# Kernel tuning notes

Measured on AMD Instinct MI355X. Metric: run time of the kernel, lower is better.

The kernel has to match this reference:

```python
import jax, jax.numpy as jnp
import numpy as np
import math

B, T, C = 4, 2048, 1024
N = 16
D = C // N  # 64
SCALE = 1.0 / math.sqrt(C)  # weight init scale, matches 1/sqrt(in_features)


def setup_inputs() -> dict:
    key = jax.random.key(0)
    ks = jax.random.split(key, 5)
    x = jax.random.normal(ks[0], (B, T, C), dtype=jnp.float32)
    wq = jax.random.normal(ks[1], (C, C), dtype=jnp.float32) * SCALE
    wk = jax.random.normal(ks[2], (C, C), dtype=jnp.float32) * SCALE
    wv = jax.random.normal(ks[3], (C, C), dtype=jnp.float32) * SCALE
    wp = jax.random.normal(ks[4], (C, C), dtype=jnp.float32) * SCALE
    zb = jnp.zeros((C,), dtype=jnp.float32)
    return {"x": x, "wq": wq, "bq": zb, "wk": wk, "bk": zb,
            "wv": wv, "bv": zb, "wp": wp, "bp": zb}


def reference(x, wq, bq, wk, bk, wv, bv, wp, bp):
    # q/k/v projections (torch Linear: x @ W.T + b), split into heads
    q = (x @ wq.T + bq).reshape(B, T, N, D)
    k = (x @ wk.T + bk).reshape(B, T, N, D)
    v = (x @ wv.T + bv).reshape(B, T, N, D)
    # scores [B, N, T, T] with causal mask (include_query=True -> key_dim = T)
    scores = jnp.einsum('bqnd,bknd->bnqk', q, k) / math.sqrt(D)
    causal = jnp.tril(jnp.ones((T, T), dtype=bool))
    scores = jnp.where(causal[None, None], scores, -jnp.inf)
    probs = jax.nn.softmax(scores, axis=-1)
    # attention output, clamp to [-10, 10] (drop_p = 0, head_mask = None)
    attn = jnp.einsum('bnqk,bknd->bqnd', probs, v)
    attn = jnp.clip(attn, -10.0, 10.0).reshape(B, T, C)
    out = attn @ wp.T + bp
    out = jnp.clip(out, -10.0, 10.0)
    return out
```

## Files before the change

### kernel.cpp

```cpp
#include <hip/hip_runtime.h>
#include <stdint.h>

typedef __attribute__((ext_vector_type(4))) float f32x4;
typedef __attribute__((ext_vector_type(8))) _Float16 h8;
typedef __attribute__((ext_vector_type(4))) float f4v;
typedef __attribute__((ext_vector_type(4))) _Float16 h4v;

#define B_ 4
#define T_ 2048
#define C_ 1024
#define NH 16
#define HD 64
#define M_ (B_*T_)
#define KD 1024

#define MFMA16(a, b, c) __builtin_amdgcn_mfma_f32_16x16x32_f16(a, b, c, 0, 0, 0)

#define GL2LDS16(g, l) \
  __builtin_amdgcn_global_load_lds((const __attribute__((address_space(1))) unsigned int*)(g), \
      (__attribute__((address_space(3))) unsigned int*)(unsigned int)(uintptr_t)(l), 16, 0, 0)

__global__ void cast_x_kernel(const float* __restrict__ src, _Float16* __restrict__ dst, int n4) {
  int i = blockIdx.x * blockDim.x + threadIdx.x;
  if (i < n4) {
    f4v v = ((const f4v*)src)[i];
    ((h4v*)dst)[i] = __builtin_convertvector(v, h4v);
  }
}

__device__ __forceinline__ void stage_f32_128x32(const float* src, _Float16* dst, int lane, int wav) {
  #pragma unroll
  for (int hh = 0; hh < 2; hh++) {
    int row = hh*64 + wav*16 + (lane >> 2);
    int colf = (lane & 3) * 8;
    const float* p = src + (size_t)row * KD + colf;
    f4v a = *(const f4v*)p;
    f4v b = *(const f4v*)(p + 4);
    h8 v;
    v[0]=(_Float16)a[0]; v[1]=(_Float16)a[1]; v[2]=(_Float16)a[2]; v[3]=(_Float16)a[3];
    v[4]=(_Float16)b[0]; v[5]=(_Float16)b[1]; v[6]=(_Float16)b[2]; v[7]=(_Float16)b[3];
    *(h8*)(dst + row*32 + colf) = v;
  }
}

template<int AMODE>
__global__ __launch_bounds__(256) void gemm_qkv_kernel(
    const _Float16* __restrict__ Xh, const float* __restrict__ Xf,
    const float* __restrict__ Wq, const float* __restrict__ Wk, const float* __restrict__ Wv,
    const float* __restrict__ bq, const float* __restrict__ bk, const float* __restrict__ bv,
    _Float16* __restrict__ Qo, _Float16* __restrict__ Ko, _Float16* __restrict__ Vo)
{
  __shared__ _Float16 As[128*32];
  __shared__ _Float16 Bs[128*32];
  int tid = threadIdx.x;
  int lane = tid & 63, wav = tid >> 6;
  int mb = blockIdx.x;
  int nbg = blockIdx.y;
  int sel = nbg >> 3, nb = nbg & 7;
  const float* W = sel == 0 ? Wq : (sel == 1 ? Wk : Wv);
  const float* bias = sel == 0 ? bq : (sel == 1 ? bk : bv);
  _Float16* Out = sel == 0 ? Qo : (sel == 1 ? Ko : Vo);
  int m0 = mb * 128, n0 = nb * 128;

  f32x4 acc[4][4] = {};

  int r_in = lane >> 2;
  int c8   = (lane & 3) * 8;
  int l15 = lane & 15, l4 = lane >> 4;
  int wr = (wav >> 1) * 64, wc = (wav & 1) * 64;

  for (int k0 = 0; k0 < KD; k0 += 32) {
    if (AMODE == 0) {
      GL2LDS16(Xh + (size_t)(m0 +      wav*16 + r_in)*KD + k0 + c8, As +        wav*512);
      GL2LDS16(Xh + (size_t)(m0 + 64 + wav*16 + r_in)*KD + k0 + c8, As + 2048 + wav*512);
    } else {
      stage_f32_128x32(Xf + (size_t)m0 * KD + k0, As, lane, wav);
    }
    stage_f32_128x32(W + (size_t)n0 * KD + k0, Bs, lane, wav);
    __syncthreads();

    h8 af[4], bf[4];
    #pragma unroll
    for (int f = 0; f < 4; f++) {
      af[f] = *(const h8*)(As + (wr + f*16 + l15)*32 + l4*8);
      bf[f] = *(const h8*)(Bs + (wc + f*16 + l15)*32 + l4*8);
    }
    #pragma unroll
    for (int i = 0; i < 4; i++)
      #pragma unroll
      for (int j = 0; j < 4; j++)
        acc[i][j] = MFMA16(af[i], bf[j], acc[i][j]);
    __syncthreads();
  }

  if (sel == 2) {
    #pragma unroll
    for (int i = 0; i < 4; i++) {
      int mrow = m0 + wr + i*16 + l4*4;
      int bb = mrow >> 11, t = mrow & 2047;
      #pragma unroll
      for (int j = 0; j < 4; j++) {
        int ncol = n0 + wc + j*16 + l15;
        float bval = bias[ncol];
        int hh = ncol >> 6, d = ncol & 63;
        h4v v;
        #pragma unroll
        for (int r = 0; r < 4; r++) v[r] = (_Float16)(acc[i][j][r] + bval);
        *(h4v*)(Vo + ((size_t)(bb*NH + hh)*HD + d)*T_ + t) = v;
      }
    }
  } else {
    #pragma unroll
    for (int i = 0; i < 4; i++) {
      int mrow = m0 + wr + i*16 + l4*4;
      #pragma unroll
      for (int j = 0; j < 4; j++) {
        int ncol = n0 + wc + j*16 + l15;
        float bval = bias[ncol];
        #pragma unroll
        for (int r = 0; r < 4; r++)
          Out[(size_t)(mrow + r)*C_ + ncol] = (_Float16)(acc[i][j][r] + bval);
      }
    }
  }
}

__global__ __launch_bounds__(256) void gemm_proj_kernel(
    const _Float16* __restrict__ A, const float* __restrict__ W,
    const float* __restrict__ bias, float* __restrict__ Out)
{
  __shared__ _Float16 As[128*32];
  __shared__ _Float16 Bs[128*32];
  int tid = threadIdx.x;
  int lane = tid & 63, wav = tid >> 6;
  int m0 = blockIdx.x * 128, n0 = blockIdx.y * 128;

  f32x4 acc[4][4] = {};
  int r_in = lane >> 2;
  int c8   = (lane & 3) * 8;
  int l15 = lane & 15, l4 = lane >> 4;
  int wr = (wav >> 1) * 64, wc = (wav & 1) * 64;

  for (int k0 = 0; k0 < KD; k0 += 32) {
    GL2LDS16(A + (size_t)(m0 +      wav*16 + r_in)*KD + k0 + c8, As +        wav*512);
    GL2LDS16(A + (size_t)(m0 + 64 + wav*16 + r_in)*KD + k0 + c8, As + 2048 + wav*512);
    stage_f32_128x32(W + (size_t)n0 * KD + k0, Bs, lane, wav);
    __syncthreads();

    h8 af[4], bf[4];
    #pragma unroll
    for (int f = 0; f < 4; f++) {
      af[f] = *(const h8*)(As + (wr + f*16 + l15)*32 + l4*8);
      bf[f] = *(const h8*)(Bs + (wc + f*16 + l15)*32 + l4*8);
    }
    #pragma unroll
    for (int i = 0; i < 4; i++)
      #pragma unroll
      for (int j = 0; j < 4; j++)
        acc[i][j] = MFMA16(af[i], bf[j], acc[i][j]);
    __syncthreads();
  }

  #pragma unroll
  for (int i = 0; i < 4; i++) {
    int mrow = m0 + wr + i*16 + l4*4;
    #pragma unroll
    for (int j = 0; j < 4; j++) {
      int ncol = n0 + wc + j*16 + l15;
      float bval = bias[ncol];
      #pragma unroll
      for (int r = 0; r < 4; r++) {
        float v = acc[i][j][r] + bval;
        v = fminf(10.f, fmaxf(-10.f, v));
        Out[(size_t)(mrow + r)*C_ + ncol] = v;
      }
    }
  }
}

__global__ __launch_bounds__(64) void attn_kernel(
    const _Float16* Q, const _Float16* __restrict__ K,
    const _Float16* __restrict__ Vt, _Float16* O)
{
  __shared__ _Float16 Plds[2*16*40];
  int lane = threadIdx.x & 63;
  int p = blockIdx.x;
  int t  = 63 - (p >> 6);
  int bh = p & 63;
  int b = bh >> 4, h = bh & 15;
  int l15 = lane & 15, l4 = lane >> 4;
  _Float16* PlA = &Plds[0];
  _Float16* PlB = &Plds[640];
  const _Float16* Kbh = K + (size_t)b*T_*C_ + h*HD;
  const _Float16* Vbh = Vt + (size_t)(b*NH + h)*HD*T_;

  int q0 = t * 32;
  int qa = q0 + l15;
  int qb = q0 + 16 + l15;

  const _Float16* qbase0 = Q + (size_t)(b*T_ + qa)*C_ + h*HD;
  const _Float16* qbase1 = Q + (size_t)(b*T_ + qb)*C_ + h*HD;
  h8 qf00 = *(const h8*)(qbase0 + l4*8);
  h8 qf01 = *(const h8*)(qbase0 + 32 + l4*8);
  h8 qf10 = *(const h8*)(qbase1 + l4*8);
  h8 qf11 = *(const h8*)(qbase1 + 32 + l4*8);

  f32x4 accA[4] = {}, accB[4] = {};
  float mA = -INFINITY, lA = 0.f;
  float mB = -INFINITY, lB = 0.f;
  int last = q0;

  h8 kf0 = *(const h8*)(Kbh + (size_t)l15*C_ + l4*8);
  h8 kf1 = *(const h8*)(Kbh + (size_t)l15*C_ + 32 + l4*8);
  h8 kf2 = *(const h8*)(Kbh + (size_t)(16 + l15)*C_ + l4*8);
  h8 kf3 = *(const h8*)(Kbh + (size_t)(16 + l15)*C_ + 32 + l4*8);

  #pragma unroll 1
  for (int kb = 0; kb <= last; kb += 32) {
    h8 vf0 = *(const h8*)(Vbh + (size_t)(l15     )*T_ + kb + l4*8);
    h8 vf1 = *(const h8*)(Vbh + (size_t)(16 + l15)*T_ + kb + l4*8);
    h8 vf2 = *(const h8*)(Vbh + (size_t)(32 + l15)*T_ + kb + l4*8);
    h8 vf3 = *(const h8*)(Vbh + (size_t)(48 + l15)*T_ + kb + l4*8);

    f32x4 s0a = {}, s1a = {}, s0b = {}, s1b = {};
    s0a = MFMA16(kf0, qf00, s0a); s0a = MFMA16(kf1, qf01, s0a);
    s1a = MFMA16(kf2, qf00, s1a); s1a = MFMA16(kf3, qf01, s1a);
    s0b = MFMA16(kf0, qf10, s0b); s0b = MFMA16(kf1, qf11, s0b);
    s1b = MFMA16(kf2, qf10, s1b); s1b = MFMA16(kf3, qf11, s1b);

    if (kb < last) {
      const _Float16* kn = Kbh + (size_t)(kb + 32)*C_;
      kf0 = *(const h8*)(kn + (size_t)l15*C_ + l4*8);
      kf1 = *(const h8*)(kn + (size_t)l15*C_ + 32 + l4*8);
      kf2 = *(const h8*)(kn + (size_t)(16 + l15)*C_ + l4*8);
      kf3 = *(const h8*)(kn + (size_t)(16 + l15)*C_ + 32 + l4*8);
    }

    float scA[8], scB[8];
    #pragma unroll
    for (int j = 0; j < 4; j++) { scA[j] = s0a[j]*0.125f; scA[4+j] = s1a[j]*0.125f; }
    #pragma unroll
    for (int j = 0; j < 4; j++) { scB[j] = s0b[j]*0.125f; scB[4+j] = s1b[j]*0.125f; }
    if (kb == last) {
      #pragma unroll
      for (int r = 0; r < 4; r++) {
        if (kb      + l4*4 + r > qa) scA[r]   = -INFINITY;
        if (kb + 16 + l4*4 + r > qa) scA[4+r] = -INFINITY;
        if (kb + 16 + l4*4 + r > qb) scB[4+r] = -INFINITY;
      }
    }
    float mxA = scA[0], mxB = scB[0];
    #pragma unroll
    for (int j = 1; j < 8; j++) { mxA = fmaxf(mxA, scA[j]); mxB = fmaxf(mxB, scB[j]); }
    mxA = fmaxf(mxA, __shfl_xor(mxA, 16)); mxB = fmaxf(mxB, __shfl_xor(mxB, 16));
    mxA = fmaxf(mxA, __shfl_xor(mxA, 32)); mxB = fmaxf(mxB, __shfl_xor(mxB, 32));
    float mnA = fmaxf(mA, mxA),        mnB = fmaxf(mB, mxB);
    float alA = __expf(mA - mnA),      alB = __expf(mB - mnB);
    mA = mnA; mB = mnB;
    float lsA = 0.f, lsB = 0.f;
    h4v pw0a, pw1a, pw0b, pw1b;
    #pragma unroll
    for (int j = 0; j < 4; j++) {
      float e;
      e = __expf(scA[j]   - mnA); lsA += e; pw0a[j] = (_Float16)e;
      e = __expf(scA[4+j] - mnA); lsA += e; pw1a[j] = (_Float16)e;
      e = __expf(scB[j]   - mnB); lsB += e; pw0b[j] = (_Float16)e;
      e = __expf(scB[4+j] - mnB); lsB += e; pw1b[j] = (_Float16)e;
    }
    lsA += __shfl_xor(lsA, 16); lsB += __shfl_xor(lsB, 16);
    lsA += __shfl_xor(lsA, 32); lsB += __shfl_xor(lsB, 32);
    lA = lA*alA + lsA; lB = lB*alB + lsB;

    *(h4v*)(PlA + l15*40 +      l4*4) = pw0a;
    *(h4v*)(PlA + l15*40 + 16 + l4*4) = pw1a;
    *(h4v*)(PlB + l15*40 +      l4*4) = pw0b;
    *(h4v*)(PlB + l15*40 + 16 + l4*4) = pw1b;

    float avA[4], avB[4];
    #pragma unroll
    for (int r = 0; r < 4; r++) { avA[r] = __shfl(alA, l4*4 + r); avB[r] = __shfl(alB, l4*4 + r); }
    #pragma unroll
    for (int c2 = 0; c2 < 4; c2++) {
      accA[c2][0] *= avA[0]; accA[c2][1] *= avA[1]; accA[c2][2] *= avA[2]; accA[c2][3] *= avA[3];
      accB[c2][0] *= avB[0]; accB[c2][1] *= avB[1]; accB[c2][2] *= avB[2]; accB[c2][3] *= avB[3];
    }

    h8 paA = *(const h8*)(PlA + l15*40 + l4*8);
    h8 paB = *(const h8*)(PlB + l15*40 + l4*8);
    accA[0] = MFMA16(paA, vf0, accA[0]);
    accA[1] = MFMA16(paA, vf1, accA[1]);
    accA[2] = MFMA16(paA, vf2, accA[2]);
    accA[3] = MFMA16(paA, vf3, accA[3]);
    accB[0] = MFMA16(paB, vf0, accB[0]);
    accB[1] = MFMA16(paB, vf1, accB[1]);
    accB[2] = MFMA16(paB, vf2, accB[2]);
    accB[3] = MFMA16(paB, vf3, accB[3]);
  }

  float lrA[4], lrB[4];
  #pragma unroll
  for (int r = 0; r < 4; r++) { lrA[r] = __shfl(lA, l4*4 + r); lrB[r] = __shfl(lB, l4*4 + r); }
  #pragma unroll
  for (int c2 = 0; c2 < 4; c2++) {
    #pragma unroll
    for (int r = 0; r < 4; r++) {
      float va = accA[c2][r] / lrA[r];
      float vb = accB[c2][r] / lrB[r];
      va = fminf(10.f, fmaxf(-10.f, va));
      vb = fminf(10.f, fmaxf(-10.f, vb));
      O[(size_t)(b*T_ + q0      + l4*4 + r)*C_ + h*HD + c2*16 + l15] = (_Float16)va;
      O[(size_t)(b*T_ + q0 + 16 + l4*4 + r)*C_ + h*HD + c2*16 + l15] = (_Float16)vb;
    }
  }
}

extern "C" void kernel_launch(void* const* d_in, const int* in_sizes, int n_in,
                              void* d_out, int out_size, void* d_ws, size_t ws_size,
                              hipStream_t stream) {
  (void)in_sizes; (void)n_in; (void)out_size;
  const float* x  = (const float*)d_in[0];
  const float* wq = (const float*)d_in[1];
  const float* bq = (const float*)d_in[2];
  const float* wk = (const float*)d_in[3];
  const float* bk = (const float*)d_in[4];
  const float* wv = (const float*)d_in[5];
  const float* bv = (const float*)d_in[6];
  const float* wp = (const float*)d_in[7];
  const float* bp = (const float*)d_in[8];
  float* out = (float*)d_out;

  char* ws = (char*)d_ws;
  const size_t MB = 1ull << 20;
  _Float16* qh = (_Float16*)(ws + 0*MB);
  _Float16* kh = (_Float16*)(ws + 16*MB);
  _Float16* vh = (_Float16*)(ws + 32*MB);
  _Float16* xh = (_Float16*)(ws + 48*MB);

  bool use_xh = ws_size >= 64*MB;
  if (use_xh) {
    cast_x_kernel<<<dim3((M_*C_/4) / 256), 256, 0, stream>>>(x, xh, M_*C_/4);
    gemm_qkv_kernel<0><<<dim3(M_/128, 24), 256, 0, stream>>>(
        xh, nullptr, wq, wk, wv, bq, bk, bv, qh, kh, vh);
  } else {
    gemm_qkv_kernel<1><<<dim3(M_/128, 24), 256, 0, stream>>>(
        nullptr, x, wq, wk, wv, bq, bk, bv, qh, kh, vh);
  }
  attn_kernel<<<dim3(64*64), 64, 0, stream>>>(qh, kh, vh, qh);
  gemm_proj_kernel<<<dim3(M_/128, C_/128), 256, 0, stream>>>(qh, wp, bp, out);
}
```

Measured before the change: 240.6 us.

## Restructure attention: paired causal tiles, 64-key blocks, exp2 and lazy rescale

The attention kernel now processes two query tiles per block, pairing tile t with tile 63-t so that causal work is balanced across blocks, and the grid is halved to match. Each loop iteration covers 64 keys instead of 32, which halves the iteration count and the per-iteration softmax overhead. The softmax scale and log2(e) are folded into Q, so exp2 replaces expf. The running-max rescale of the accumulator is skipped unless the new max exceeds the old by more than 8, and probabilities are packed with cvt_pkrtz. In exchange the kernel uses more registers, and the round-toward-zero packing and deferred rescale slightly change numerics.

After: 239.0 us. Within noise of the previous version (-0.7%).

```diff
diff --git a/kernel.cpp b/kernel.cpp
--- a/kernel.cpp
+++ b/kernel.cpp
@@ -15,6 +15,23 @@
 #define KD 1024
 
 #define MFMA16(a, b, c) __builtin_amdgcn_mfma_f32_16x16x32_f16(a, b, c, 0, 0, 0)
+
+#if __has_builtin(__builtin_amdgcn_exp2f)
+#define EXP2(x) __builtin_amdgcn_exp2f(x)
+#else
+#define EXP2(x) exp2f(x)
+#endif
+
+#if __has_builtin(__builtin_amdgcn_cvt_pkrtz)
+static __device__ __forceinline__ unsigned pk16(float a, float b) {
+  return __builtin_bit_cast(unsigned, __builtin_amdgcn_cvt_pkrtz(a, b));
+}
+#else
+static __device__ __forceinline__ unsigned pk16(float a, float b) {
+  union { _Float16 h[2]; unsigned u; } x;
+  x.h[0] = (_Float16)a; x.h[1] = (_Float16)b; return x.u;
+}
+#endif
 
 #define GL2LDS16(g, l) \
   __builtin_amdgcn_global_load_lds((const __attribute__((address_space(1))) unsigned int*)(g), \
@@ -182,136 +199,157 @@
     const _Float16* Q, const _Float16* __restrict__ K,
     const _Float16* __restrict__ Vt, _Float16* O)
 {
-  __shared__ _Float16 Plds[2*16*40];
+  __shared__ _Float16 Plds[2][16*72];
   int lane = threadIdx.x & 63;
   int p = blockIdx.x;
-  int t  = 63 - (p >> 6);
+  int pair = p >> 6;
   int bh = p & 63;
   int b = bh >> 4, h = bh & 15;
   int l15 = lane & 15, l4 = lane >> 4;
-  _Float16* PlA = &Plds[0];
-  _Float16* PlB = &Plds[640];
+  _Float16* PlA = &Plds[0][0];
+  _Float16* PlB = &Plds[1][0];
   const _Float16* Kbh = K + (size_t)b*T_*C_ + h*HD;
   const _Float16* Vbh = Vt + (size_t)(b*NH + h)*HD*T_;
-
-  int q0 = t * 32;
-  int qa = q0 + l15;
-  int qb = q0 + 16 + l15;
-
-  const _Float16* qbase0 = Q + (size_t)(b*T_ + qa)*C_ + h*HD;
-  const _Float16* qbase1 = Q + (size_t)(b*T_ + qb)*C_ + h*HD;
-  h8 qf00 = *(const h8*)(qbase0 + l4*8);
-  h8 qf01 = *(const h8*)(qbase0 + 32 + l4*8);
-  h8 qf10 = *(const h8*)(qbase1 + l4*8);
-  h8 qf11 = *(const h8*)(qbase1 + 32 + l4*8);
-
-  f32x4 accA[4] = {}, accB[4] = {};
-  float mA = -INFINITY, lA = 0.f;
-  float mB = -INFINITY, lB = 0.f;
-  int last = q0;
-
-  h8 kf0 = *(const h8*)(Kbh + (size_t)l15*C_ + l4*8);
-  h8 kf1 = *(const h8*)(Kbh + (size_t)l15*C_ + 32 + l4*8);
-  h8 kf2 = *(const h8*)(Kbh + (size_t)(16 + l15)*C_ + l4*8);
-  h8 kf3 = *(const h8*)(Kbh + (size_t)(16 + l15)*C_ + 32 + l4*8);
+  const _Float16 QSC = (_Float16)0.18033688011f;
+
+#define CHAIN(sv, qrow, m, lp, acc, Pl)                                        \
+  {                                                                            \
+    float sc[16];                                                              \
+    _Pragma("unroll") for (int g = 0; g < 4; g++) {                            \
+      sc[g*4+0] = sv[g][0]; sc[g*4+1] = sv[g][1];                              \
+      sc[g*4+2] = sv[g][2]; sc[g*4+3] = sv[g][3];                              \
+    }                                                                          \
+    if (kb == lastb) {                                                         \
+      _Pragma("unroll") for (int g = 0; g < 4; g++)                            \
+        _Pragma("unroll") for (int r = 0; r < 4; r++)                          \
+          if (kb + g*16 + l4*4 + r > (qrow)) sc[g*4+r] = -INFINITY;            \
+    }                                                                          \
+    float mx = sc[0];                                                          \
+    _Pragma("unroll") for (int j = 1; j < 16; j++) mx = fmaxf(mx, sc[j]);      \
+    mx = fmaxf(mx, __shfl_xor(mx, 16));                                        \
+    mx = fmaxf(mx, __shfl_xor(mx, 32));                                        \
+    if (__any(mx > (m) + 8.f)) {                                               \
+      float mn = fmaxf((m), mx);                                               \
+      float al = EXP2((m) - mn);                                               \
+      (lp) *= al;                                                              \
+      float av0 = __shfl(al, l4*4+0), av1 = __shfl(al, l4*4+1);                \
+      float av2 = __shfl(al, l4*4+2), av3 = __shfl(al, l4*4+3);                \
+      _Pragma("unroll") for (int c2 = 0; c2 < 4; c2++) {                       \
+        acc[c2][0] *= av0; acc[c2][1] *= av1;                                  \
+        acc[c2][2] *= av2; acc[c2][3] *= av3;                                  \
+      }                                                                        \
+      (m) = mn;                                                                \
+    }                                                                          \
+    _Pragma("unroll") for (int g = 0; g < 4; g++) {                            \
+      float e0 = EXP2(sc[g*4+0] - (m)), e1 = EXP2(sc[g*4+1] - (m));            \
+      float e2 = EXP2(sc[g*4+2] - (m)), e3 = EXP2(sc[g*4+3] - (m));            \
+      (lp) += (e0 + e1) + (e2 + e3);                                           \
+      uint2 u; u.x = pk16(e0, e1); u.y = pk16(e2, e3);                         \
+      *(uint2*)((Pl) + l15*72 + g*16 + l4*4) = u;                              \
+    }                                                                          \
+  }
 
   #pragma unroll 1
-  for (int kb = 0; kb <= last; kb += 32) {
-    h8 vf0 = *(const h8*)(Vbh + (size_t)(l15     )*T_ + kb + l4*8);
-    h8 vf1 = *(const h8*)(Vbh + (size_t)(16 + l15)*T_ + kb + l4*8);
-    h8 vf2 = *(const h8*)(Vbh + (size_t)(32 + l15)*T_ + kb + l4*8);
-    h8 vf3 = *(const h8*)(Vbh + (size_t)(48 + l15)*T_ + kb + l4*8);
-
-    f32x4 s0a = {}, s1a = {}, s0b = {}, s1b = {};
-    s0a = MFMA16(kf0, qf00, s0a); s0a = MFMA16(kf1, qf01, s0a);
-    s1a = MFMA16(kf2, qf00, s1a); s1a = MFMA16(kf3, qf01, s1a);
-    s0b = MFMA16(kf0, qf10, s0b); s0b = MFMA16(kf1, qf11, s0b);
-    s1b = MFMA16(kf2, qf10, s1b); s1b = MFMA16(kf3, qf11, s1b);
-
-    if (kb < last) {
-      const _Float16* kn = Kbh + (size_t)(kb + 32)*C_;
-      kf0 = *(const h8*)(kn + (size_t)l15*C_ + l4*8);
-      kf1 = *(const h8*)(kn + (size_t)l15*C_ + 32 + l4*8);
-      kf2 = *(const h8*)(kn + (size_t)(16 + l15)*C_ + l4*8);
-      kf3 = *(const h8*)(kn + (size_t)(16 + l15)*C_ + 32 + l4*8);
-    }
-
-    float scA[8], scB[8];
-    #pragma unroll
-    for (int j = 0; j < 4; j++) { scA[j] = s0a[j]*0.125f; scA[4+j] = s1a[j]*0.125f; }
-    #pragma unroll
-    for (int j = 0; j < 4; j++) { scB[j] = s0b[j]*0.125f; scB[4+j] = s1b[j]*0.125f; }
-    if (kb == last) {
+  for (int ti = 0; ti < 2; ti++) {
+    int t = ti ? (63 - pair) : pair;
+    int q0 = t * 32;
+    int qa = q0 + l15, qb = q0 + 16 + l15;
+
+    const _Float16* qp0 = Q + (size_t)(b*T_ + qa)*C_ + h*HD;
+    const _Float16* qp1 = Q + (size_t)(b*T_ + qb)*C_ + h*HD;
+    h8 qf00 = *(const h8*)(qp0 + l4*8)      * QSC;
+    h8 qf01 = *(const h8*)(qp0 + 32 + l4*8) * QSC;
+    h8 qf10 = *(const h8*)(qp1 + l4*8)      * QSC;
+    h8 qf11 = *(const h8*)(qp1 + 32 + l4*8) * QSC;
+
+    f32x4 accA[4] = {}, accB[4] = {};
+    float mA = -INFINITY, lAp = 0.f;
+    float mB = -INFINITY, lBp = 0.f;
+    int lastb = (q0 >> 6) << 6;
+
+    h8 kf0, kf1, kf2, kf3, kf4, kf5, kf6, kf7;
+    kf0 = *(const h8*)(Kbh + (size_t)(     l15)*C_ + l4*8);
+    kf1 = *(const h8*)(Kbh + (size_t)(     l15)*C_ + 32 + l4*8);
+    kf2 = *(const h8*)(Kbh + (size_t)(16 + l15)*C_ + l4*8);
+    kf3 = *(const h8*)(Kbh + (size_t)(16 + l15)*C_ + 32 + l4*8);
+    kf4 = *(const h8*)(Kbh + (size_t)(32 + l15)*C_ + l4*8);
+    kf5 = *(const h8*)(Kbh + (size_t)(32 + l15)*C_ + 32 + l4*8);
+    kf6 = *(const h8*)(Kbh + (size_t)(48 + l15)*C_ + l4*8);
+    kf7 = *(const h8*)(Kbh + (size_t)(48 + l15)*C_ + 32 + l4*8);
+
+    #pragma unroll 1
+    for (int kb = 0; kb <= lastb; kb += 64) {
+      h8 vf00 = *(const h8*)(Vbh + (size_t)(     l15)*T_ + kb + l4*8);
+      h8 vf01 = *(const h8*)(Vbh + (size_t)(     l15)*T_ + kb + 32 + l4*8);
+      h8 vf10 = *(const h8*)(Vbh + (size_t)(16 + l15)*T_ + kb + l4*8);
+      h8 vf11 = *(const h8*)(Vbh + (size_t)(16 + l15)*T_ + kb + 32 + l4*8);
+      h8 vf20 = *(const h8*)(Vbh + (size_t)(32 + l15)*T_ + kb + l4*8);
+      h8 vf21 = *(const h8*)(Vbh + (size_t)(32 + l15)*T_ + kb + 32 + l4*8);
+      h8 vf30 = *(const h8*)(Vbh + (size_t)(48 + l15)*T_ + kb + l4*8);
+      h8 vf31 = *(const h8*)(Vbh + (size_t)(48 + l15)*T_ + kb + 32 + l4*8);
+
+      f32x4 z = {};
+      f32x4 sA[4], sB[4];
+      sA[0] = MFMA16(kf1, qf01, MFMA16(kf0, qf00, z));
+      sA[1] = MFMA16(kf3, qf01, MFMA16(kf2, qf00, z));
+      sA[2] = MFMA16(kf5, qf01, MFMA16(kf4, qf00, z));
+      sA[3] = MFMA16(kf7, qf01, MFMA16(kf6, qf00, z));
+      sB[0] = MFMA16(kf1, qf11, MFMA16(kf0, qf10, z));
+      sB[1] = MFMA16(kf3, qf11, MFMA16(kf2, qf10, z));
+      sB[2] = MFMA16(kf5, qf11, MFMA16(kf4, qf10, z));
+      sB[3] = MFMA16(kf7, qf11, MFMA16(kf6, qf10, z));
+
+      if (kb < lastb) {
+        const _Float16* kn = Kbh + (size_t)(kb + 64)*C_;
+        kf0 = *(const h8*)(kn + (size_t)(     l15)*C_ + l4*8);
+        kf1 = *(const h8*)(kn + (size_t)(     l15)*C_ + 32 + l4*8);
+        kf2 = *(const h8*)(kn + (size_t)(16 + l15)*C_ + l4*8);
+        kf3 = *(const h8*)(kn + (size_t)(16 + l15)*C_ + 32 + l4*8);
+        kf4 = *(const h8*)(kn + (size_t)(32 + l15)*C_ + l4*8);
+        kf5 = *(const h8*)(kn + (size_t)(32 + l15)*C_ + 32 + l4*8);
+        kf6 = *(const h8*)(kn + (size_t)(48 + l15)*C_ + l4*8);
+        kf7 = *(const h8*)(kn + (size_t)(48 + l15)*C_ + 32 + l4*8);
+      }
+
+      CHAIN(sA, qa, mA, lAp, accA, PlA)
+      CHAIN(sB, qb, mB, lBp, accB, PlB)
+
+      h8 paA0 = *(const h8*)(PlA + l15*72 + l4*8);
+      h8 paA1 = *(const h8*)(PlA + l15*72 + 32 + l4*8);
+      h8 paB0 = *(const h8*)(PlB + l15*72 + l4*8);
+      h8 paB1 = *(const h8*)(PlB + l15*72 + 32 + l4*8);
+      accA[0] = MFMA16(paA1, vf01, MFMA16(paA0, vf00, accA[0]));
+      accA[1] = MFMA16(paA1, vf11, MFMA16(paA0, vf10, accA[1]));
+      accA[2] = MFMA16(paA1, vf21, MFMA16(paA0, vf20, accA[2]));
+      accA[3] = MFMA16(paA1, vf31, MFMA16(paA0, vf30, accA[3]));
+      accB[0] = MFMA16(paB1, vf01, MFMA16(paB0, vf00, accB[0]));
+      accB[1] = MFMA16(paB1, vf11, MFMA16(paB0, vf10, accB[1]));
+      accB[2] = MFMA16(paB1, vf21, MFMA16(paB0, vf20, accB[2]));
+      accB[3] = MFMA16(paB1, vf31, MFMA16(paB0, vf30, accB[3]));
+    }
+
+    lAp += __shfl_xor(lAp, 16); lAp += __shfl_xor(lAp, 32);
+    lBp += __shfl_xor(lBp, 16); lBp += __shfl_xor(lBp, 32);
+    float lrA[4], lrB[4];
+    #pragma unroll
+    for (int r = 0; r < 4; r++) {
+      lrA[r] = 1.f / __shfl(lAp, l4*4 + r);
+      lrB[r] = 1.f / __shfl(lBp, l4*4 + r);
+    }
+    #pragma unroll
+    for (int c2 = 0; c2 < 4; c2++) {
       #pragma unroll
       for (int r = 0; r < 4; r++) {
-        if (kb      + l4*4 + r > qa) scA[r]   = -INFINITY;
-        if (kb + 16 + l4*4 + r > qa) scA[4+r] = -INFINITY;
-        if (kb + 16 + l4*4 + r > qb) scB[4+r] = -INFINITY;
-      }
-    }
-    float mxA = scA[0], mxB = scB[0];
-    #pragma unroll
-    for (int j = 1; j < 8; j++) { mxA = fmaxf(mxA, scA[j]); mxB = fmaxf(mxB, scB[j]); }
-    mxA = fmaxf(mxA, __shfl_xor(mxA, 16)); mxB = fmaxf(mxB, __shfl_xor(mxB, 16));
-    mxA = fmaxf(mxA, __shfl_xor(mxA, 32)); mxB = fmaxf(mxB, __shfl_xor(mxB, 32));
-    float mnA = fmaxf(mA, mxA),        mnB = fmaxf(mB, mxB);
-    float alA = __expf(mA - mnA),      alB = __expf(mB - mnB);
-    mA = mnA; mB = mnB;
-    float lsA = 0.f, lsB = 0.f;
-    h4v pw0a, pw1a, pw0b, pw1b;
-    #pragma unroll
-    for (int j = 0; j < 4; j++) {
-      float e;
-      e = __expf(scA[j]   - mnA); lsA += e; pw0a[j] = (_Float16)e;
-      e = __expf(scA[4+j] - mnA); lsA += e; pw1a[j] = (_Float16)e;
-      e = __expf(scB[j]   - mnB); lsB += e; pw0b[j] = (_Float16)e;
-      e = __expf(scB[4+j] - mnB); lsB += e; pw1b[j] = (_Float16)e;
-    }
-    lsA += __shfl_xor(lsA, 16); lsB += __shfl_xor(lsB, 16);
-    lsA += __shfl_xor(lsA, 32); lsB += __shfl_xor(lsB, 32);
-    lA = lA*alA + lsA; lB = lB*alB + lsB;
-
-    *(h4v*)(PlA + l15*40 +      l4*4) = pw0a;
-    *(h4v*)(PlA + l15*40 + 16 + l4*4) = pw1a;
-    *(h4v*)(PlB + l15*40 +      l4*4) = pw0b;
-    *(h4v*)(PlB + l15*40 + 16 + l4*4) = pw1b;
-
-    float avA[4], avB[4];
-    #pragma unroll
-    for (int r = 0; r < 4; r++) { avA[r] = __shfl(alA, l4*4 + r); avB[r] = __shfl(alB, l4*4 + r); }
-    #pragma unroll
-    for (int c2 = 0; c2 < 4; c2++) {
-      accA[c2][0] *= avA[0]; accA[c2][1] *= avA[1]; accA[c2][2] *= avA[2]; accA[c2][3] *= avA[3];
-      accB[c2][0] *= avB[0]; accB[c2][1] *= avB[1]; accB[c2][2] *= avB[2]; accB[c2][3] *= avB[3];
-    }
-
-    h8 paA = *(const h8*)(PlA + l15*40 + l4*8);
-    h8 paB = *(const h8*)(PlB + l15*40 + l4*8);
-    accA[0] = MFMA16(paA, vf0, accA[0]);
-    accA[1] = MFMA16(paA, vf1, accA[1]);
-    accA[2] = MFMA16(paA, vf2, accA[2]);
-    accA[3] = MFMA16(paA, vf3, accA[3]);
-    accB[0] = MFMA16(paB, vf0, accB[0]);
-    accB[1] = MFMA16(paB, vf1, accB[1]);
-    accB[2] = MFMA16(paB, vf2, accB[2]);
-    accB[3] = MFMA16(paB, vf3, accB[3]);
-  }
-
-  float lrA[4], lrB[4];
-  #pragma unroll
-  for (int r = 0; r < 4; r++) { lrA[r] = __shfl(lA, l4*4 + r); lrB[r] = __shfl(lB, l4*4 + r); }
-  #pragma unroll
-  for (int c2 = 0; c2 < 4; c2++) {
-    #pragma unroll
-    for (int r = 0; r < 4; r++) {
-      float va = accA[c2][r] / lrA[r];
-      float vb = accB[c2][r] / lrB[r];
-      va = fminf(10.f, fmaxf(-10.f, va));
-      vb = fminf(10.f, fmaxf(-10.f, vb));
-      O[(size_t)(b*T_ + q0      + l4*4 + r)*C_ + h*HD + c2*16 + l15] = (_Float16)va;
-      O[(size_t)(b*T_ + q0 + 16 + l4*4 + r)*C_ + h*HD + c2*16 + l15] = (_Float16)vb;
-    }
-  }
+        float va = accA[c2][r] * lrA[r];
+        float vb = accB[c2][r] * lrB[r];
+        va = fminf(10.f, fmaxf(-10.f, va));
+        vb = fminf(10.f, fmaxf(-10.f, vb));
+        O[(size_t)(b*T_ + q0      + l4*4 + r)*C_ + h*HD + c2*16 + l15] = (_Float16)va;
+        O[(size_t)(b*T_ + q0 + 16 + l4*4 + r)*C_ + h*HD + c2*16 + l15] = (_Float16)vb;
+      }
+    }
+  }
+#undef CHAIN
 }
 
 extern "C" void kernel_launch(void* const* d_in, const int* in_sizes, int n_in,
@@ -345,6 +383,6 @@
     gemm_qkv_kernel<1><<<dim3(M_/128, 24), 256, 0, stream>>>(
         nullptr, x, wq, wk, wv, bq, bk, bv, qh, kh, vh);
   }
-  attn_kernel<<<dim3(64*64), 64, 0, stream>>>(qh, kh, vh, qh);
+  attn_kernel<<<dim3(2048), 64, 0, stream>>>(qh, kh, vh, qh);
   gemm_proj_kernel<<<dim3(M_/128, C_/128), 256, 0, stream>>>(qh, wp, bp, out);
 }
```
